# Kernel optimization log

Hardware: AMD Instinct MI355X
Metric: run time of the kernel (lower is better)

Reference implementation:

```python
import jax, jax.numpy as jnp
import numpy as np


def setup_inputs() -> dict:
    key = jax.random.key(0)
    k1, k2, k3 = jax.random.split(key, 3)
    B, P, E, H = 256, 512, 256, 128
    x = jax.random.normal(k1, (B, P, E), dtype=jnp.float32)
    # torch Linear weights are [out, in]; init uniform(-0.1, 0.1)
    w1 = jax.random.uniform(k2, (H, E), minval=-0.1, maxval=0.1, dtype=jnp.float32)
    w2 = jax.random.uniform(k3, (1, H), minval=-0.1, maxval=0.1, dtype=jnp.float32)
    return {"x": x, "w1": w1, "w2": w2}


def reference(x, w1, w2):
    # scores: [B, P] = tanh(x @ w1.T) @ w2.T
    h = jnp.tanh(jnp.einsum('bpe,he->bph', x, w1))
    scores = jnp.einsum('bph,h->bp', h, w2[0])
    weight = jax.nn.softmax(scores, axis=1)            # softmax over pool dim
    pooled = jnp.einsum('bp,bpe->be', weight, x)       # weighted-sum pool
    return pooled
```

## Files before the change

### kernel.cpp

```cpp
#include <hip/hip_runtime.h>

#define NB 256
#define NP 512
#define NE 256
#define NH 128
#define PT 64
#define NT (NP / PT)
#define RS 264

typedef __attribute__((ext_vector_type(8))) short bf16x8;
typedef __attribute__((ext_vector_type(4))) short short4v;
typedef __attribute__((ext_vector_type(4))) float f32x4;

__device__ __forceinline__ short f2bf(float f) {
  union { float f; unsigned u; } v; v.f = f;
  unsigned r = v.u + 0x7fffu + ((v.u >> 16) & 1u);
  return (short)(r >> 16);
}
__device__ __forceinline__ float bf2f(short s) {
  union { unsigned u; float f; } v;
  v.u = ((unsigned)(unsigned short)s) << 16;
  return v.f;
}
__device__ __forceinline__ float fast_tanh(float x) {
  float u = __builtin_amdgcn_exp2f(x * 2.8853900817779268f);
  return 1.0f - 2.0f * __builtin_amdgcn_rcpf(u + 1.0f);
}

__global__ __launch_bounds__(512, 2) void pathattn_kernel(
    const float* __restrict__ x, const float* __restrict__ w1,
    const float* __restrict__ w2, float* __restrict__ out) {
  __shared__ short xs[2][PT * RS];
  __shared__ float sp[2][PT];
  __shared__ float expw[PT];
  __shared__ float pool2[2][NE];
  __shared__ float zarr[PT];

  const int tid  = threadIdx.x;
  const int lane = tid & 63;
  const int wid  = tid >> 6;
  const int jg   = wid & 1;
  const int h    = wid >> 1;
  const int b    = blockIdx.x;
  const float* xb = x + (size_t)b * NP * NE;

  bf16x8 bfrag[4][8];
  float w2v[4];
  {
    const int n  = lane & 15;
    const int kg = lane >> 4;
    #pragma unroll
    for (int jt = 0; jt < 4; ++jt) {
      const int j = jg * 64 + jt * 16 + n;
      w2v[jt] = w2[j];
      #pragma unroll
      for (int kt = 0; kt < 8; ++kt) {
        const f32x4* s = (const f32x4*)(w1 + j * NE + kt * 32 + kg * 8);
        f32x4 a = s[0], c = s[1];
        bf16x8 v;
        v[0]=f2bf(a[0]); v[1]=f2bf(a[1]); v[2]=f2bf(a[2]); v[3]=f2bf(a[3]);
        v[4]=f2bf(c[0]); v[5]=f2bf(c[1]); v[6]=f2bf(c[2]); v[7]=f2bf(c[3]);
        bfrag[jt][kt] = v;
      }
    }
  }

  f32x4 streg[8];
  auto issue_loads = [&](int tile) {
    const float* base = xb + tile * PT * NE;
    #pragma unroll
    for (int rr = 0; rr < 8; ++rr) {
      int f   = rr * 512 + tid;
      int row = f >> 6;
      int c4  = f & 63;
      streg[rr] = *(const f32x4*)(base + row * NE + c4 * 4);
    }
  };
  auto write_tile = [&](int buf) {
    #pragma unroll
    for (int rr = 0; rr < 8; ++rr) {
      int f   = rr * 512 + tid;
      int row = f >> 6;
      int c4  = f & 63;
      short4v v;
      v[0]=f2bf(streg[rr][0]); v[1]=f2bf(streg[rr][1]);
      v[2]=f2bf(streg[rr][2]); v[3]=f2bf(streg[rr][3]);
      *(short4v*)(&xs[buf][row * RS + c4 * 4]) = v;
    }
  };

  issue_loads(0);
  write_tile(0);
  __syncthreads();

  float pacc = 0.f;
  float zacc = 0.f;
  const int pe = tid & 255;
  const int pq = tid >> 8;

  for (int t = 0; t < NT; ++t) {
    const int cur = t & 1;
    if (t + 1 < NT) issue_loads(t + 1);

    f32x4 acc[4];
    #pragma unroll
    for (int jt = 0; jt < 4; ++jt) acc[jt] = (f32x4){0.f,0.f,0.f,0.f};
    const int arow = h * 16 + (lane & 15);
    const int akg  = (lane >> 4) * 8;
    #pragma unroll
    for (int kt = 0; kt < 8; ++kt) {
      bf16x8 av = *(const bf16x8*)(&xs[cur][arow * RS + kt * 32 + akg]);
      #pragma unroll
      for (int jt = 0; jt < 4; ++jt)
        acc[jt] = __builtin_amdgcn_mfma_f32_16x16x32_bf16(av, bfrag[jt][kt], acc[jt], 0, 0, 0);
    }
    float sc[4] = {0.f, 0.f, 0.f, 0.f};
    #pragma unroll
    for (int jt = 0; jt < 4; ++jt) {
      #pragma unroll
      for (int r = 0; r < 4; ++r)
        sc[r] += fast_tanh(acc[jt][r]) * w2v[jt];
    }
    #pragma unroll
    for (int m = 1; m <= 8; m <<= 1) {
      #pragma unroll
      for (int r = 0; r < 4; ++r) sc[r] += __shfl_xor(sc[r], m, 64);
    }
    if ((lane & 15) == 0) {
      const int rbase = h * 16 + (lane >> 4) * 4;
      #pragma unroll
      for (int r = 0; r < 4; ++r) sp[jg][rbase + r] = sc[r];
    }
    __syncthreads();

    if (tid < PT) {
      float s = sp[0][tid] + sp[1][tid];
      float e = __builtin_amdgcn_exp2f(s * 1.4426950408889634f);
      expw[tid] = e;
      zacc += e;
    }
    __syncthreads();

    #pragma unroll
    for (int pp = 0; pp < 32; ++pp) {
      const int p = pq * 32 + pp;
      pacc += expw[p] * bf2f(xs[cur][p * RS + pe]);
    }

    if (t + 1 < NT) {
      write_tile(cur ^ 1);
      __syncthreads();
    }
  }

  pool2[pq][pe] = pacc;
  if (tid < PT) zarr[tid] = zacc;
  __syncthreads();
  if (tid < NE) {
    float z = 0.f;
    #pragma unroll
    for (int i = 0; i < PT; ++i) z += zarr[i];
    float v = pool2[0][tid] + pool2[1][tid];
    out[(size_t)b * NE + tid] = v / z;
  }
}

extern "C" void kernel_launch(void* const* d_in, const int* in_sizes, int n_in,
                              void* d_out, int out_size, void* d_ws, size_t ws_size,
                              hipStream_t stream) {
  (void)in_sizes; (void)n_in; (void)out_size; (void)d_ws; (void)ws_size;
  const float* x  = (const float*)d_in[0];
  const float* w1 = (const float*)d_in[1];
  const float* w2 = (const float*)d_in[2];
  float* out = (float*)d_out;
  pathattn_kernel<<<NB, 512, 0, stream>>>(x, w1, w2, out);
}
```

Measured before the change: 47.05 us.

## Split pool dimension across two blocks per batch and combine partial softmax sums

```diff
diff --git a/kernel.cpp b/kernel.cpp
--- a/kernel.cpp
+++ b/kernel.cpp
@@ -5,7 +5,8 @@
 #define NE 256
 #define NH 128
 #define PT 64
-#define NT (NP / PT)
+#define HALF 256
+#define NT (HALF / PT)
 #define RS 264
 
 typedef __attribute__((ext_vector_type(8))) short bf16x8;
@@ -27,41 +28,37 @@
   return 1.0f - 2.0f * __builtin_amdgcn_rcpf(u + 1.0f);
 }
 
-__global__ __launch_bounds__(512, 2) void pathattn_kernel(
+__global__ __launch_bounds__(512, 4) void pathattn_part(
     const float* __restrict__ x, const float* __restrict__ w1,
-    const float* __restrict__ w2, float* __restrict__ out) {
+    const float* __restrict__ w2, float* __restrict__ wsPool,
+    float* __restrict__ wsZ) {
   __shared__ short xs[2][PT * RS];
-  __shared__ float sp[2][PT];
+  __shared__ float sp[8][PT];
   __shared__ float expw[PT];
   __shared__ float pool2[2][NE];
-  __shared__ float zarr[PT];
 
   const int tid  = threadIdx.x;
   const int lane = tid & 63;
   const int wid  = tid >> 6;
-  const int jg   = wid & 1;
-  const int h    = wid >> 1;
-  const int b    = blockIdx.x;
-  const float* xb = x + (size_t)b * NP * NE;
+  const int b    = blockIdx.x >> 1;
+  const int half = blockIdx.x & 1;
+  const float* xb = x + (size_t)b * NP * NE + (size_t)half * HALF * NE;
 
-  bf16x8 bfrag[4][8];
-  float w2v[4];
+  bf16x8 bfrag[8];
+  float w2v;
+  const int n15 = lane & 15;
+  const int kg8 = (lane >> 4) * 8;
   {
-    const int n  = lane & 15;
-    const int kg = lane >> 4;
+    const int j = wid * 16 + n15;
+    w2v = w2[j];
     #pragma unroll
-    for (int jt = 0; jt < 4; ++jt) {
-      const int j = jg * 64 + jt * 16 + n;
-      w2v[jt] = w2[j];
-      #pragma unroll
-      for (int kt = 0; kt < 8; ++kt) {
-        const f32x4* s = (const f32x4*)(w1 + j * NE + kt * 32 + kg * 8);
-        f32x4 a = s[0], c = s[1];
-        bf16x8 v;
-        v[0]=f2bf(a[0]); v[1]=f2bf(a[1]); v[2]=f2bf(a[2]); v[3]=f2bf(a[3]);
-        v[4]=f2bf(c[0]); v[5]=f2bf(c[1]); v[6]=f2bf(c[2]); v[7]=f2bf(c[3]);
-        bfrag[jt][kt] = v;
-      }
+    for (int kt = 0; kt < 8; ++kt) {
+      const f32x4* s = (const f32x4*)(w1 + j * NE + kt * 32 + kg8);
+      f32x4 a = s[0], c = s[1];
+      bf16x8 v;
+      v[0]=f2bf(a[0]); v[1]=f2bf(a[1]); v[2]=f2bf(a[2]); v[3]=f2bf(a[3]);
+      v[4]=f2bf(c[0]); v[5]=f2bf(c[1]); v[6]=f2bf(c[2]); v[7]=f2bf(c[3]);
+      bfrag[kt] = v;
     }
   }
 
@@ -104,37 +101,42 @@
 
     f32x4 acc[4];
     #pragma unroll
-    for (int jt = 0; jt < 4; ++jt) acc[jt] = (f32x4){0.f,0.f,0.f,0.f};
-    const int arow = h * 16 + (lane & 15);
-    const int akg  = (lane >> 4) * 8;
+    for (int rt = 0; rt < 4; ++rt) acc[rt] = (f32x4){0.f,0.f,0.f,0.f};
     #pragma unroll
     for (int kt = 0; kt < 8; ++kt) {
-      bf16x8 av = *(const bf16x8*)(&xs[cur][arow * RS + kt * 32 + akg]);
       #pragma unroll
-      for (int jt = 0; jt < 4; ++jt)
-        acc[jt] = __builtin_amdgcn_mfma_f32_16x16x32_bf16(av, bfrag[jt][kt], acc[jt], 0, 0, 0);
+      for (int rt = 0; rt < 4; ++rt) {
+        bf16x8 av = *(const bf16x8*)(&xs[cur][(rt*16 + n15) * RS + kt*32 + kg8]);
+        acc[rt] = __builtin_amdgcn_mfma_f32_16x16x32_bf16(av, bfrag[kt], acc[rt], 0, 0, 0);
+      }
     }
-    float sc[4] = {0.f, 0.f, 0.f, 0.f};
+    float sc[4][4];
     #pragma unroll
-    for (int jt = 0; jt < 4; ++jt) {
+    for (int rt = 0; rt < 4; ++rt)
       #pragma unroll
       for (int r = 0; r < 4; ++r)
-        sc[r] += fast_tanh(acc[jt][r]) * w2v[jt];
-    }
+        sc[rt][r] = fast_tanh(acc[rt][r]) * w2v;
     #pragma unroll
-    for (int m = 1; m <= 8; m <<= 1) {
+    for (int m = 1; m <= 8; m <<= 1)
       #pragma unroll
-      for (int r = 0; r < 4; ++r) sc[r] += __shfl_xor(sc[r], m, 64);
-    }
-    if ((lane & 15) == 0) {
-      const int rbase = h * 16 + (lane >> 4) * 4;
+      for (int rt = 0; rt < 4; ++rt)
+        #pragma unroll
+        for (int r = 0; r < 4; ++r)
+          sc[rt][r] += __shfl_xor(sc[rt][r], m, 64);
+    if (n15 == 0) {
       #pragma unroll
-      for (int r = 0; r < 4; ++r) sp[jg][rbase + r] = sc[r];
+      for (int rt = 0; rt < 4; ++rt) {
+        const int rbase = rt * 16 + (lane >> 4) * 4;
+        #pragma unroll
+        for (int r = 0; r < 4; ++r) sp[wid][rbase + r] = sc[rt][r];
+      }
     }
     __syncthreads();
 
     if (tid < PT) {
-      float s = sp[0][tid] + sp[1][tid];
+      float s = 0.f;
+      #pragma unroll
+      for (int w = 0; w < 8; ++w) s += sp[w][tid];
       float e = __builtin_amdgcn_exp2f(s * 1.4426950408889634f);
       expw[tid] = e;
       zacc += e;
@@ -154,24 +156,37 @@
   }
 
   pool2[pq][pe] = pacc;
-  if (tid < PT) zarr[tid] = zacc;
+  float z = zacc;
+  if (wid == 0) {
+    #pragma unroll
+    for (int m = 1; m <= 32; m <<= 1) z += __shfl_xor(z, m, 64);
+  }
   __syncthreads();
-  if (tid < NE) {
-    float z = 0.f;
-    #pragma unroll
-    for (int i = 0; i < PT; ++i) z += zarr[i];
-    float v = pool2[0][tid] + pool2[1][tid];
-    out[(size_t)b * NE + tid] = v / z;
-  }
+  if (tid < NE)
+    wsPool[(size_t)blockIdx.x * NE + tid] = pool2[0][tid] + pool2[1][tid];
+  if (tid == 0)
+    wsZ[blockIdx.x] = z;
+}
+
+__global__ void pathattn_combine(const float* __restrict__ wsPool,
+                                 const float* __restrict__ wsZ,
+                                 float* __restrict__ out) {
+  const int b = blockIdx.x, e = threadIdx.x;
+  float v = wsPool[(size_t)(2*b) * NE + e] + wsPool[(size_t)(2*b+1) * NE + e];
+  float z = wsZ[2*b] + wsZ[2*b+1];
+  out[(size_t)b * NE + e] = v / z;
 }
 
 extern "C" void kernel_launch(void* const* d_in, const int* in_sizes, int n_in,
                               void* d_out, int out_size, void* d_ws, size_t ws_size,
                               hipStream_t stream) {
-  (void)in_sizes; (void)n_in; (void)out_size; (void)d_ws; (void)ws_size;
+  (void)in_sizes; (void)n_in; (void)out_size; (void)ws_size;
   const float* x  = (const float*)d_in[0];
   const float* w1 = (const float*)d_in[1];
   const float* w2 = (const float*)d_in[2];
   float* out = (float*)d_out;
-  pathattn_kernel<<<NB, 512, 0, stream>>>(x, w1, w2, out);
+  float* wsPool = (float*)d_ws;
+  float* wsZ    = wsPool + 512 * NE;
+  pathattn_part<<<2 * NB, 512, 0, stream>>>(x, w1, w2, wsPool, wsZ);
+  pathattn_combine<<<NB, NE, 0, stream>>>(wsPool, wsZ, out);
 }
```

Result: faster. 45.84 us (-2.6%).
